# Performance work log

Hardware: AMD Instinct MI355X
Metric: run time of the kernel (lower is better)

## Reference

```python
import jax, jax.numpy as jnp
import numpy as np
from jax import lax

K = 3  # kernel_size


def setup_inputs() -> dict:
    key = jax.random.key(0)
    k1, k2 = jax.random.split(key)
    image = jax.random.normal(k1, (1, 1, 8192, 8192), dtype=jnp.float32)
    # original module: torch.randint(0, 2, (k, k)) -> 0/1 kernel
    kernel = jax.random.randint(k2, (K, K), 0, 2).astype(jnp.float32)
    return {"image": image, "kernel": kernel}


def reference(image, kernel):
    # Faithful math: zero-pad by k//2, then sliding-window cross-correlation
    # sum(window * kernel). For odd k the original loop bounds
    # (H_pad - (k//2 + 1)) equal H_pad - k + 1, i.e. a VALID conv on the
    # padded image (== 'same' conv on the original image).
    k = kernel.shape[0]
    p = k // 2
    x = jnp.pad(image, ((0, 0), (0, 0), (p, p), (p, p)))  # [N,C,Hp,Wp]
    w = kernel[None, None, :, :]  # [O=1, I=1, k, k]
    out = lax.conv_general_dilated(
        x, w, window_strides=(1, 1), padding='VALID',
        dimension_numbers=('NCHW', 'OIHW', 'NCHW'))
    return out  # [1, 1, 8192, 8192]
```

## Files before the change

kernel.cpp:

```cpp
#include <hip/hip_runtime.h>

#define IMG_H 8192
#define IMG_W 8192
#define TILE_W 256
#define TILE_H 32
#define ST_ROWS (TILE_H + 2)
#define ST_COLS 264
#define CHUNKS_PER_ROW (ST_COLS / 4)
#define N_CHUNKS (ST_ROWS * CHUNKS_PER_ROW)
#define GRID_X (IMG_W / TILE_W)
#define GRID_Y (IMG_H / TILE_H)

typedef float floatx4 __attribute__((ext_vector_type(4)));

__global__ __launch_bounds__(256) void conv3x3_lds(const float* __restrict__ img,
                                                   const float* __restrict__ ker,
                                                   float* __restrict__ out) {
    __shared__ float lds[ST_ROWS * ST_COLS];

    const int bx = blockIdx.x & (GRID_X - 1);
    const int by = blockIdx.x >> 5;
    const int X0 = bx * TILE_W;
    const int Y0 = by * TILE_H;
    const int t  = threadIdx.x;

    #pragma unroll
    for (int pass = 0; pass < 9; ++pass) {
        const int chunk = pass * 256 + t;
        if (chunk < N_CHUNKS) {
            const int r  = chunk / CHUNKS_PER_ROW;
            const int c4 = chunk % CHUNKS_PER_ROW;
            int gy = Y0 - 1 + r;
            gy = min(max(gy, 0), IMG_H - 1);
            int gx = X0 - 4 + c4 * 4;
            gx = min(max(gx, 0), IMG_W - 4);
            const float* src = img + (size_t)gy * IMG_W + gx;
            float* dst = &lds[chunk * 4];
            __builtin_amdgcn_global_load_lds(
                (const __attribute__((address_space(1))) void*)src,
                (__attribute__((address_space(3))) void*)dst,
                16, 0, 0);
        }
    }
    asm volatile("s_waitcnt vmcnt(0)" ::: "memory");
    __syncthreads();

    const bool eT = (Y0 == 0), eB = (Y0 == IMG_H - TILE_H);
    const bool eL = (X0 == 0), eR = (X0 == IMG_W - TILE_W);
    if (eT | eB | eL | eR) {
        const floatx4 z = {0.f, 0.f, 0.f, 0.f};
        if (eT && t < CHUNKS_PER_ROW) *(floatx4*)&lds[t * 4] = z;
        if (eB && t < CHUNKS_PER_ROW) *(floatx4*)&lds[(ST_ROWS - 1) * ST_COLS + t * 4] = z;
        if (eL && t < ST_ROWS) *(floatx4*)&lds[t * ST_COLS + 0] = z;
        if (eR && t < ST_ROWS) *(floatx4*)&lds[t * ST_COLS + 260] = z;
        __syncthreads();
    }

    const float w00 = ker[0], w01 = ker[1], w02 = ker[2];
    const float w10 = ker[3], w11 = ker[4], w12 = ker[5];
    const float w20 = ker[6], w21 = ker[7], w22 = ker[8];

    const int wv = t >> 6;
    const int ln = t & 63;
    const int oyBase = wv * 8;
    const int colBase = 4 * ln;

    #define LDROW(r, A, B, C) do {                                     \
        const float* p_ = &lds[(r) * ST_COLS + colBase];               \
        A = *(const floatx4*)p_;                                       \
        B = *(const floatx4*)(p_ + 4);                                 \
        C = *(const floatx4*)(p_ + 8);                                 \
    } while (0)

    floatx4 a0, b0, c0, a1, b1, c1;
    LDROW(oyBase + 0, a0, b0, c0);
    LDROW(oyBase + 1, a1, b1, c1);

    #pragma unroll
    for (int oy = 0; oy < 8; ++oy) {
        floatx4 a2, b2, c2;
        LDROW(oyBase + oy + 2, a2, b2, c2);

        float t0[6] = {a0.w, b0.x, b0.y, b0.z, b0.w, c0.x};
        float t1[6] = {a1.w, b1.x, b1.y, b1.z, b1.w, c1.x};
        float t2[6] = {a2.w, b2.x, b2.y, b2.z, b2.w, c2.x};

        floatx4 res;
        #pragma unroll
        for (int j = 0; j < 4; ++j) {
            res[j] = w00 * t0[j] + w01 * t0[j + 1] + w02 * t0[j + 2]
                   + w10 * t1[j] + w11 * t1[j + 1] + w12 * t1[j + 2]
                   + w20 * t2[j] + w21 * t2[j + 1] + w22 * t2[j + 2];
        }

        const int y = Y0 + oyBase + oy;
        __builtin_nontemporal_store(res, (floatx4*)(out + (size_t)y * IMG_W + X0 + colBase));

        a0 = a1; b0 = b1; c0 = c1;
        a1 = a2; b1 = b2; c1 = c2;
    }
    #undef LDROW
}

extern "C" void kernel_launch(void* const* d_in, const int* in_sizes, int n_in,
                              void* d_out, int out_size, void* d_ws, size_t ws_size,
                              hipStream_t stream) {
    const float* img = (const float*)d_in[0];
    const float* ker = (const float*)d_in[1];
    float* out = (float*)d_out;

    const int grid = GRID_X * GRID_Y;
    conv3x3_lds<<<grid, 256, 0, stream>>>(img, ker, out);
}
```

Before: 89.80 us.

## Split interior tile loads into two phases and overlap with compute

For interior blocks, the global-to-LDS loads are issued in two groups, and the kernel waits only on the first group (s_waitcnt vmcnt(4)) before computing the top half of the tile. The second half is computed after another barrier, so load latency can overlap with compute inside the block. Interior blocks also drop the coordinate clamping. Each wave now handles two 4-row strips instead of one 8-row strip. The second wait relies on how vmcnt counts the interleaved nontemporal stores, which makes correctness and gain depend on hardware counter ordering.

```diff
diff --git a/kernel.cpp b/kernel.cpp
--- a/kernel.cpp
+++ b/kernel.cpp
@@ -13,6 +13,39 @@
 
 typedef float floatx4 __attribute__((ext_vector_type(4)));
 
+#define LDROW(r, A, B, C) do {                                     \
+    const float* p_ = &lds[(r) * ST_COLS + colBase];               \
+    A = *(const floatx4*)p_;                                       \
+    B = *(const floatx4*)(p_ + 4);                                 \
+    C = *(const floatx4*)(p_ + 8);                                 \
+} while (0)
+
+#define COMPUTE4(oyBase_) do {                                                        \
+    const int oyB = (oyBase_);                                                        \
+    floatx4 a0, b0, c0, a1, b1, c1;                                                   \
+    LDROW(oyB + 0, a0, b0, c0);                                                       \
+    LDROW(oyB + 1, a1, b1, c1);                                                       \
+    _Pragma("unroll")                                                                 \
+    for (int oy = 0; oy < 4; ++oy) {                                                  \
+        floatx4 a2, b2, c2;                                                           \
+        LDROW(oyB + oy + 2, a2, b2, c2);                                              \
+        float t0[6] = {a0.w, b0.x, b0.y, b0.z, b0.w, c0.x};                           \
+        float t1[6] = {a1.w, b1.x, b1.y, b1.z, b1.w, c1.x};                           \
+        float t2[6] = {a2.w, b2.x, b2.y, b2.z, b2.w, c2.x};                           \
+        floatx4 res;                                                                  \
+        _Pragma("unroll")                                                             \
+        for (int j = 0; j < 4; ++j) {                                                 \
+            res[j] = w00 * t0[j] + w01 * t0[j + 1] + w02 * t0[j + 2]                  \
+                   + w10 * t1[j] + w11 * t1[j + 1] + w12 * t1[j + 2]                  \
+                   + w20 * t2[j] + w21 * t2[j + 1] + w22 * t2[j + 2];                 \
+        }                                                                             \
+        const int y_ = Y0 + oyB + oy;                                                 \
+        __builtin_nontemporal_store(res, (floatx4*)(out + (size_t)y_ * IMG_W + X0 + colBase)); \
+        a0 = a1; b0 = b1; c0 = c1;                                                    \
+        a1 = a2; b1 = b2; c1 = c2;                                                    \
+    }                                                                                 \
+} while (0)
+
 __global__ __launch_bounds__(256) void conv3x3_lds(const float* __restrict__ img,
                                                    const float* __restrict__ ker,
                                                    float* __restrict__ out) {
@@ -24,82 +57,84 @@
     const int Y0 = by * TILE_H;
     const int t  = threadIdx.x;
 
-    #pragma unroll
-    for (int pass = 0; pass < 9; ++pass) {
-        const int chunk = pass * 256 + t;
-        if (chunk < N_CHUNKS) {
-            const int r  = chunk / CHUNKS_PER_ROW;
-            const int c4 = chunk % CHUNKS_PER_ROW;
-            int gy = Y0 - 1 + r;
-            gy = min(max(gy, 0), IMG_H - 1);
-            int gx = X0 - 4 + c4 * 4;
-            gx = min(max(gx, 0), IMG_W - 4);
-            const float* src = img + (size_t)gy * IMG_W + gx;
-            float* dst = &lds[chunk * 4];
-            __builtin_amdgcn_global_load_lds(
-                (const __attribute__((address_space(1))) void*)src,
-                (__attribute__((address_space(3))) void*)dst,
-                16, 0, 0);
-        }
-    }
-    asm volatile("s_waitcnt vmcnt(0)" ::: "memory");
-    __syncthreads();
+    const float w00 = ker[0], w01 = ker[1], w02 = ker[2];
+    const float w10 = ker[3], w11 = ker[4], w12 = ker[5];
+    const float w20 = ker[6], w21 = ker[7], w22 = ker[8];
+
+    const int wv = t >> 6;
+    const int ln = t & 63;
+    const int colBase = 4 * ln;
 
     const bool eT = (Y0 == 0), eB = (Y0 == IMG_H - TILE_H);
     const bool eL = (X0 == 0), eR = (X0 == IMG_W - TILE_W);
-    if (eT | eB | eL | eR) {
+
+    if (!(eT | eB | eL | eR)) {
+        #pragma unroll
+        for (int pass = 0; pass < 5; ++pass) {
+            const int chunk = pass * 256 + t;
+            const int r  = chunk / CHUNKS_PER_ROW;
+            const int c4 = chunk % CHUNKS_PER_ROW;
+            const float* src = img + (size_t)(Y0 - 1 + r) * IMG_W + (X0 - 4 + c4 * 4);
+            __builtin_amdgcn_global_load_lds(
+                (const __attribute__((address_space(1))) void*)src,
+                (__attribute__((address_space(3))) void*)&lds[chunk * 4], 16, 0, 0);
+        }
+        __builtin_amdgcn_sched_barrier(0);
+        #pragma unroll
+        for (int pass = 5; pass < 9; ++pass) {
+            const int chunk = pass * 256 + t;
+            if (chunk < N_CHUNKS) {
+                const int r  = chunk / CHUNKS_PER_ROW;
+                const int c4 = chunk % CHUNKS_PER_ROW;
+                const float* src = img + (size_t)(Y0 - 1 + r) * IMG_W + (X0 - 4 + c4 * 4);
+                __builtin_amdgcn_global_load_lds(
+                    (const __attribute__((address_space(1))) void*)src,
+                    (__attribute__((address_space(3))) void*)&lds[chunk * 4], 16, 0, 0);
+            }
+        }
+        __builtin_amdgcn_sched_barrier(0);
+        asm volatile("s_waitcnt vmcnt(4)" ::: "memory");
+        __builtin_amdgcn_s_barrier();
+        __builtin_amdgcn_sched_barrier(0);
+
+        COMPUTE4(4 * wv);
+
+        __builtin_amdgcn_sched_barrier(0);
+        asm volatile("s_waitcnt vmcnt(4)" ::: "memory");
+        __builtin_amdgcn_s_barrier();
+        __builtin_amdgcn_sched_barrier(0);
+
+        COMPUTE4(16 + 4 * wv);
+    } else {
+        #pragma unroll
+        for (int pass = 0; pass < 9; ++pass) {
+            const int chunk = pass * 256 + t;
+            if (chunk < N_CHUNKS) {
+                const int r  = chunk / CHUNKS_PER_ROW;
+                const int c4 = chunk % CHUNKS_PER_ROW;
+                int gy = Y0 - 1 + r;
+                gy = min(max(gy, 0), IMG_H - 1);
+                int gx = X0 - 4 + c4 * 4;
+                gx = min(max(gx, 0), IMG_W - 4);
+                const float* src = img + (size_t)gy * IMG_W + gx;
+                __builtin_amdgcn_global_load_lds(
+                    (const __attribute__((address_space(1))) void*)src,
+                    (__attribute__((address_space(3))) void*)&lds[chunk * 4], 16, 0, 0);
+            }
+        }
+        asm volatile("s_waitcnt vmcnt(0)" ::: "memory");
+        __syncthreads();
+
         const floatx4 z = {0.f, 0.f, 0.f, 0.f};
         if (eT && t < CHUNKS_PER_ROW) *(floatx4*)&lds[t * 4] = z;
         if (eB && t < CHUNKS_PER_ROW) *(floatx4*)&lds[(ST_ROWS - 1) * ST_COLS + t * 4] = z;
         if (eL && t < ST_ROWS) *(floatx4*)&lds[t * ST_COLS + 0] = z;
         if (eR && t < ST_ROWS) *(floatx4*)&lds[t * ST_COLS + 260] = z;
         __syncthreads();
+
+        COMPUTE4(4 * wv);
+        COMPUTE4(16 + 4 * wv);
     }
-
-    const float w00 = ker[0], w01 = ker[1], w02 = ker[2];
-    const float w10 = ker[3], w11 = ker[4], w12 = ker[5];
-    const float w20 = ker[6], w21 = ker[7], w22 = ker[8];
-
-    const int wv = t >> 6;
-    const int ln = t & 63;
-    const int oyBase = wv * 8;
-    const int colBase = 4 * ln;
-
-    #define LDROW(r, A, B, C) do {                                     \
-        const float* p_ = &lds[(r) * ST_COLS + colBase];               \
-        A = *(const floatx4*)p_;                                       \
-        B = *(const floatx4*)(p_ + 4);                                 \
-        C = *(const floatx4*)(p_ + 8);                                 \
-    } while (0)
-
-    floatx4 a0, b0, c0, a1, b1, c1;
-    LDROW(oyBase + 0, a0, b0, c0);
-    LDROW(oyBase + 1, a1, b1, c1);
-
-    #pragma unroll
-    for (int oy = 0; oy < 8; ++oy) {
-        floatx4 a2, b2, c2;
-        LDROW(oyBase + oy + 2, a2, b2, c2);
-
-        float t0[6] = {a0.w, b0.x, b0.y, b0.z, b0.w, c0.x};
-        float t1[6] = {a1.w, b1.x, b1.y, b1.z, b1.w, c1.x};
-        float t2[6] = {a2.w, b2.x, b2.y, b2.z, b2.w, c2.x};
-
-        floatx4 res;
-        #pragma unroll
-        for (int j = 0; j < 4; ++j) {
-            res[j] = w00 * t0[j] + w01 * t0[j + 1] + w02 * t0[j + 2]
-                   + w10 * t1[j] + w11 * t1[j + 1] + w12 * t1[j + 2]
-                   + w20 * t2[j] + w21 * t2[j + 1] + w22 * t2[j + 2];
-        }
-
-        const int y = Y0 + oyBase + oy;
-        __builtin_nontemporal_store(res, (floatx4*)(out + (size_t)y * IMG_W + X0 + colBase));
-
-        a0 = a1; b0 = b1; c0 = c1;
-        a1 = a2; b1 = b2; c1 = c2;
-    }
-    #undef LDROW
 }
 
 extern "C" void kernel_launch(void* const* d_in, const int* in_sizes, int n_in,
```

Measured after the change: 90.93 us. Within noise of the previous version (+1.3%).

## Process multiple row tiles per block with double-buffered LDS prefetch

Applied to the files above, without the earlier changes.

Each block now processes 8 vertically stacked 32-row tiles instead of one, so the grid shrinks by 8x. The next tile is staged into a second LDS buffer with global_load_lds while the current tile is computed, and a partial vmcnt wait plus a barrier hands the buffers over. The aim is to hide global-load latency behind compute and cut per-block launch and setup overhead. The cost is doubled LDS per block, which lowers occupancy, and a reliance on vmcnt ordering between the pending loads and the interleaved nontemporal stores.

```diff
diff --git a/kernel.cpp b/kernel.cpp
--- a/kernel.cpp
+++ b/kernel.cpp
@@ -8,98 +8,122 @@
 #define ST_COLS 264
 #define CHUNKS_PER_ROW (ST_COLS / 4)
 #define N_CHUNKS (ST_ROWS * CHUNKS_PER_ROW)
+#define K_TILES 8
 #define GRID_X (IMG_W / TILE_W)
-#define GRID_Y (IMG_H / TILE_H)
+#define GRID_YG (IMG_H / (TILE_H * K_TILES))
 
 typedef float floatx4 __attribute__((ext_vector_type(4)));
 
-__global__ __launch_bounds__(256) void conv3x3_lds(const float* __restrict__ img,
-                                                   const float* __restrict__ ker,
-                                                   float* __restrict__ out) {
-    __shared__ float lds[ST_ROWS * ST_COLS];
+__global__ __launch_bounds__(256) void conv3x3_pipe(const float* __restrict__ img,
+                                                    const float* __restrict__ ker,
+                                                    float* __restrict__ out) {
+    __shared__ float ldsA[ST_ROWS * ST_COLS];
+    __shared__ float ldsB[ST_ROWS * ST_COLS];
 
-    const int bx = blockIdx.x & (GRID_X - 1);
-    const int by = blockIdx.x >> 5;
-    const int X0 = bx * TILE_W;
-    const int Y0 = by * TILE_H;
-    const int t  = threadIdx.x;
+    const int bx  = blockIdx.x & (GRID_X - 1);
+    const int byg = blockIdx.x >> 5;
+    const int X0  = bx * TILE_W;
+    const int Y0b = byg * (TILE_H * K_TILES);
+    const int t   = threadIdx.x;
+    const int wv  = t >> 6;
+    const int ln  = t & 63;
+    const int colBase = 4 * ln;
 
-    #pragma unroll
-    for (int pass = 0; pass < 9; ++pass) {
-        const int chunk = pass * 256 + t;
-        if (chunk < N_CHUNKS) {
-            const int r  = chunk / CHUNKS_PER_ROW;
-            const int c4 = chunk % CHUNKS_PER_ROW;
-            int gy = Y0 - 1 + r;
-            gy = min(max(gy, 0), IMG_H - 1);
-            int gx = X0 - 4 + c4 * 4;
-            gx = min(max(gx, 0), IMG_W - 4);
-            const float* src = img + (size_t)gy * IMG_W + gx;
-            float* dst = &lds[chunk * 4];
-            __builtin_amdgcn_global_load_lds(
-                (const __attribute__((address_space(1))) void*)src,
-                (__attribute__((address_space(3))) void*)dst,
-                16, 0, 0);
-        }
-    }
-    asm volatile("s_waitcnt vmcnt(0)" ::: "memory");
-    __syncthreads();
-
-    const bool eT = (Y0 == 0), eB = (Y0 == IMG_H - TILE_H);
     const bool eL = (X0 == 0), eR = (X0 == IMG_W - TILE_W);
-    if (eT | eB | eL | eR) {
-        const floatx4 z = {0.f, 0.f, 0.f, 0.f};
-        if (eT && t < CHUNKS_PER_ROW) *(floatx4*)&lds[t * 4] = z;
-        if (eB && t < CHUNKS_PER_ROW) *(floatx4*)&lds[(ST_ROWS - 1) * ST_COLS + t * 4] = z;
-        if (eL && t < ST_ROWS) *(floatx4*)&lds[t * ST_COLS + 0] = z;
-        if (eR && t < ST_ROWS) *(floatx4*)&lds[t * ST_COLS + 260] = z;
-        __syncthreads();
-    }
 
     const float w00 = ker[0], w01 = ker[1], w02 = ker[2];
     const float w10 = ker[3], w11 = ker[4], w12 = ker[5];
     const float w20 = ker[6], w21 = ker[7], w22 = ker[8];
 
-    const int wv = t >> 6;
-    const int ln = t & 63;
-    const int oyBase = wv * 8;
-    const int colBase = 4 * ln;
+    auto stage = [&](float* buf, int Y0_) {
+        #pragma unroll
+        for (int pass = 0; pass < 9; ++pass) {
+            const int chunk = pass * 256 + t;
+            if (chunk < N_CHUNKS) {
+                const int r  = chunk / CHUNKS_PER_ROW;
+                const int c4 = chunk - r * CHUNKS_PER_ROW;
+                int gy = Y0_ - 1 + r;  gy = min(max(gy, 0), IMG_H - 1);
+                int gx = X0 - 4 + c4 * 4;  gx = min(max(gx, 0), IMG_W - 4);
+                __builtin_amdgcn_global_load_lds(
+                    (const __attribute__((address_space(1))) void*)(img + (size_t)gy * IMG_W + gx),
+                    (__attribute__((address_space(3))) void*)(buf + chunk * 4), 16, 0, 0);
+            }
+        }
+    };
 
-    #define LDROW(r, A, B, C) do {                                     \
-        const float* p_ = &lds[(r) * ST_COLS + colBase];               \
-        A = *(const floatx4*)p_;                                       \
-        B = *(const floatx4*)(p_ + 4);                                 \
-        C = *(const floatx4*)(p_ + 8);                                 \
-    } while (0)
+    auto fixup = [&](float* buf, bool fT, bool fB) {
+        const floatx4 z = {0.f, 0.f, 0.f, 0.f};
+        if (fT && t < CHUNKS_PER_ROW) *(floatx4*)&buf[t * 4] = z;
+        if (fB && t < CHUNKS_PER_ROW) *(floatx4*)&buf[(ST_ROWS - 1) * ST_COLS + t * 4] = z;
+        if (eL && t < ST_ROWS) *(floatx4*)&buf[t * ST_COLS + 0] = z;
+        if (eR && t < ST_ROWS) *(floatx4*)&buf[t * ST_COLS + 260] = z;
+        asm volatile("s_waitcnt lgkmcnt(0)" ::: "memory");
+        __builtin_amdgcn_s_barrier();
+    };
 
-    floatx4 a0, b0, c0, a1, b1, c1;
-    LDROW(oyBase + 0, a0, b0, c0);
-    LDROW(oyBase + 1, a1, b1, c1);
+    auto compute4 = [&](const float* buf, int Y0_, int oyB) {
+        #define LDROW(r, A, B, C) do {                                   \
+            const float* p_ = &buf[(r) * ST_COLS + colBase];             \
+            A = *(const floatx4*)p_;                                     \
+            B = *(const floatx4*)(p_ + 4);                               \
+            C = *(const floatx4*)(p_ + 8);                               \
+        } while (0)
+        floatx4 a0, b0, c0, a1, b1, c1;
+        LDROW(oyB + 0, a0, b0, c0);
+        LDROW(oyB + 1, a1, b1, c1);
+        #pragma unroll
+        for (int oy = 0; oy < 4; ++oy) {
+            floatx4 a2, b2, c2;
+            LDROW(oyB + oy + 2, a2, b2, c2);
+            float t0[6] = {a0.w, b0.x, b0.y, b0.z, b0.w, c0.x};
+            float t1[6] = {a1.w, b1.x, b1.y, b1.z, b1.w, c1.x};
+            float t2[6] = {a2.w, b2.x, b2.y, b2.z, b2.w, c2.x};
+            floatx4 res;
+            #pragma unroll
+            for (int j = 0; j < 4; ++j) {
+                res[j] = w00 * t0[j] + w01 * t0[j + 1] + w02 * t0[j + 2]
+                       + w10 * t1[j] + w11 * t1[j + 1] + w12 * t1[j + 2]
+                       + w20 * t2[j] + w21 * t2[j + 1] + w22 * t2[j + 2];
+            }
+            const int y_ = Y0_ + oyB + oy;
+            __builtin_nontemporal_store(res, (floatx4*)(out + (size_t)y_ * IMG_W + X0 + colBase));
+            a0 = a1; b0 = b1; c0 = c1;
+            a1 = a2; b1 = b2; c1 = c2;
+        }
+        #undef LDROW
+    };
 
-    #pragma unroll
-    for (int oy = 0; oy < 8; ++oy) {
-        floatx4 a2, b2, c2;
-        LDROW(oyBase + oy + 2, a2, b2, c2);
+    float* cur = ldsA;
+    float* nxt = ldsB;
 
-        float t0[6] = {a0.w, b0.x, b0.y, b0.z, b0.w, c0.x};
-        float t1[6] = {a1.w, b1.x, b1.y, b1.z, b1.w, c1.x};
-        float t2[6] = {a2.w, b2.x, b2.y, b2.z, b2.w, c2.x};
+    stage(cur, Y0b);
+    asm volatile("s_waitcnt vmcnt(0)" ::: "memory");
+    __builtin_amdgcn_s_barrier();
+    __builtin_amdgcn_sched_barrier(0);
+    {
+        const bool fT = (Y0b == 0);
+        if (fT | eL | eR) fixup(cur, fT, false);
+    }
 
-        floatx4 res;
-        #pragma unroll
-        for (int j = 0; j < 4; ++j) {
-            res[j] = w00 * t0[j] + w01 * t0[j + 1] + w02 * t0[j + 2]
-                   + w10 * t1[j] + w11 * t1[j + 1] + w12 * t1[j + 2]
-                   + w20 * t2[j] + w21 * t2[j + 1] + w22 * t2[j + 2];
+    for (int tt = 0; tt < K_TILES; ++tt) {
+        const int Y0 = Y0b + tt * TILE_H;
+
+        if (tt + 1 < K_TILES) stage(nxt, Y0 + TILE_H);
+
+        compute4(cur, Y0, 4 * wv);
+        compute4(cur, Y0, 16 + 4 * wv);
+
+        if (tt + 1 < K_TILES) {
+            __builtin_amdgcn_sched_barrier(0);
+            asm volatile("s_waitcnt vmcnt(8)" ::: "memory");
+            __builtin_amdgcn_s_barrier();
+            __builtin_amdgcn_sched_barrier(0);
+            const int Y0n = Y0 + TILE_H;
+            const bool fB = (Y0n == IMG_H - TILE_H);
+            if (fB | eL | eR) fixup(nxt, false, fB);
+            float* tmp = cur; cur = nxt; nxt = tmp;
         }
-
-        const int y = Y0 + oyBase + oy;
-        __builtin_nontemporal_store(res, (floatx4*)(out + (size_t)y * IMG_W + X0 + colBase));
-
-        a0 = a1; b0 = b1; c0 = c1;
-        a1 = a2; b1 = b2; c1 = c2;
     }
-    #undef LDROW
 }
 
 extern "C" void kernel_launch(void* const* d_in, const int* in_sizes, int n_in,
@@ -109,6 +133,6 @@
     const float* ker = (const float*)d_in[1];
     float* out = (float*)d_out;
 
-    const int grid = GRID_X * GRID_Y;
-    conv3x3_lds<<<grid, 256, 0, stream>>>(img, ker, out);
+    const int grid = GRID_X * GRID_YG;
+    conv3x3_pipe<<<grid, 256, 0, stream>>>(img, ker, out);
 }
```

Measured after the change: 97.51 us. +8.6%, slower.
